# Kernel optimization log

Measured on AMD Instinct MI355X. Metric: run time of the kernel, lower is better.

## Reference

```python
import jax, jax.numpy as jnp
import numpy as np

INPUT, HIDDEN, OUTPUT = 512, 1024, 256
BATCH, SEQ = 128, 512


def setup_inputs() -> dict:
    key = jax.random.key(0)
    ks = jax.random.split(key, 8)
    s_in = 1.0 / np.sqrt(INPUT)
    s_h = 1.0 / np.sqrt(HIDDEN)
    return {
        "x": jax.random.normal(ks[0], (BATCH, SEQ, INPUT), dtype=jnp.float32),
        "W_in": jax.random.uniform(ks[1], (INPUT, HIDDEN), jnp.float32, -s_in, s_in),
        "b_in": jax.random.uniform(ks[2], (HIDDEN,), jnp.float32, -s_in, s_in),
        "W_h": jax.random.uniform(ks[3], (HIDDEN, HIDDEN), jnp.float32, -s_h, s_h),
        "b_h": jax.random.uniform(ks[4], (HIDDEN,), jnp.float32, -s_h, s_h),
        "tau": jnp.ones((HIDDEN,), jnp.float32),
        "W_out": jax.random.uniform(ks[5], (HIDDEN, OUTPUT), jnp.float32, -s_h, s_h),
        "b_out": jax.random.uniform(ks[6], (OUTPUT,), jnp.float32, -s_h, s_h),
    }


def reference(x, W_in, b_in, W_h, b_h, tau, W_out, b_out):
    # Precompute input projections for all timesteps in one big GEMM: [B,S,H]
    xin = jnp.einsum('bsi,ih->bsh', x, W_in) + b_in

    def step(h, xin_t):
        dx = jnp.tanh(xin_t + h @ W_h + b_h)
        h_new = h + (dx - h) / tau
        return h_new, None

    h0 = jnp.zeros((x.shape[0], W_h.shape[0]), x.dtype)
    h_final, _ = jax.lax.scan(step, h0, jnp.swapaxes(xin, 0, 1))
    return h_final @ W_out + b_out
```

## Files before the change

kernel.cpp:

```cpp
#include <hip/hip_runtime.h>
#include <hip/hip_fp16.h>

typedef _Float16 half8 __attribute__((ext_vector_type(8)));
typedef float floatx4 __attribute__((ext_vector_type(4)));
typedef unsigned int uintx4 __attribute__((ext_vector_type(4)));

#define INPUT  512
#define HIDDEN 1024
#define OUTPUT 256
#define BATCH  128
#define SEQ    512

__global__ __launch_bounds__(256) void transpose_f32_to_f16(
    const float* __restrict__ in, _Float16* __restrict__ out, int K, int N) {
  __shared__ float tile[32][33];
  int bi = blockIdx.x;
  int bj = blockIdx.y;
  int cc = threadIdx.x & 31;
  int rr = threadIdx.x >> 5;
#pragma unroll
  for (int s = 0; s < 4; ++s) {
    int r = rr + 8 * s;
    tile[r][cc] = in[(size_t)(bi * 32 + r) * N + bj * 32 + cc];
  }
  __syncthreads();
#pragma unroll
  for (int s = 0; s < 4; ++s) {
    int nl = rr + 8 * s;
    out[(size_t)(bj * 32 + nl) * K + bi * 32 + cc] = (_Float16)tile[cc][nl];
  }
}

__global__ __launch_bounds__(256) void pack_win(
    const float* __restrict__ W, _Float16* __restrict__ P) {
  int idx = blockIdx.x * 256 + threadIdx.x;
  int k = idx >> 10, n = idx & 1023;
  P[((size_t)(k >> 5) << 15) + (n << 5) + (k & 31)] = (_Float16)W[idx];
}

__global__ __launch_bounds__(256) void xin_gemm(
    const float* __restrict__ x, const _Float16* __restrict__ WinP,
    _Float16* __restrict__ xin) {
  int bid = blockIdx.x;
  int bm = (bid & 7) * 128 + ((bid >> 3) & 127);
  int bn = bid >> 10;
  int tid = threadIdx.x;
  int l = tid & 63;
  int w = tid >> 6;
  int l15 = l & 15;
  int lk = (l >> 4) << 3;

  int rowbase = bm * 64 + w * 16;
  int colbase = bn * 128;

  floatx4 acc[8];
#pragma unroll
  for (int nt = 0; nt < 8; ++nt) acc[nt] = (floatx4){0.f, 0.f, 0.f, 0.f};

  const float* xrow = x + (size_t)(rowbase + l15) * INPUT;

  for (int k0 = 0; k0 < INPUT; k0 += 32) {
    int ak = k0 + lk;
    float4 xa = *reinterpret_cast<const float4*>(xrow + ak);
    float4 xb = *reinterpret_cast<const float4*>(xrow + ak + 4);
    half8 a;
    a[0] = (_Float16)xa.x; a[1] = (_Float16)xa.y;
    a[2] = (_Float16)xa.z; a[3] = (_Float16)xa.w;
    a[4] = (_Float16)xb.x; a[5] = (_Float16)xb.y;
    a[6] = (_Float16)xb.z; a[7] = (_Float16)xb.w;
    const _Float16* pq = WinP + ((size_t)(k0 >> 5) << 15) + l15 * 32 + lk;
#pragma unroll
    for (int nt = 0; nt < 8; ++nt) {
      half8 b = *reinterpret_cast<const half8*>(pq + (colbase + nt * 16) * 32);
      acc[nt] = __builtin_amdgcn_mfma_f32_16x16x32_f16(a, b, acc[nt], 0, 0, 0);
    }
  }

  int orow = rowbase + ((l >> 4) << 2);
#pragma unroll
  for (int nt = 0; nt < 8; ++nt)
#pragma unroll
    for (int i = 0; i < 4; ++i) {
      int r = orow + i;
      int b = r >> 9;
      int s = r & 511;
      xin[((size_t)s * BATCH + b) * HIDDEN + colbase + nt * 16 + l15] =
          (_Float16)acc[nt][i];
    }
}

__global__ __launch_bounds__(512) void liquid_scan(
    const _Float16* __restrict__ xin,
    const _Float16* __restrict__ WhT,
    const float* __restrict__ b_in, const float* __restrict__ b_h,
    const float* __restrict__ tau,
    unsigned int* hbuf,
    float* __restrict__ hfinal) {
  int blk = blockIdx.x;
  int m = blk & 7;
  int j = blk >> 3;
  int tid = threadIdx.x;
  int l = tid & 63;
  int w = tid >> 6;
  int nt = w & 3;
  int kg = w >> 2;
  int l15 = l & 15;
  int lk = (l >> 4) << 3;

  __shared__ _Float16 Ald[16][1032];
  __shared__ float part[2][4][2][64];

  int ncol = j * 64 + nt * 16 + l15;
  half8 bfrag[16];
  {
    const _Float16* wb = WhT + (size_t)ncol * HIDDEN + kg * 512 + lk;
#pragma unroll
    for (int q = 0; q < 16; ++q)
      bfrag[q] = *reinterpret_cast<const half8*>(wb + q * 32);
  }

  float bias_c = b_in[ncol] + b_h[ncol];
  float invtau_c = 1.0f / tau[ncol];
  float hown[2] = {0.f, 0.f};
  int erow_i = (l >> 4) << 2;
  const int i0 = kg * 2;
  const int r0 = m * 16 + erow_i + i0;

  const int srow = tid >> 8;
  const int scol4 = (tid & 255) * 4;
  unsigned int* gbase = hbuf + m * 16384 + tid * 4;

  _Float16 xc[2], x1[2], xn[2];
#pragma unroll
  for (int i2 = 0; i2 < 2; ++i2) {
    xc[i2] = xin[((size_t)0 * BATCH + r0 + i2) * HIDDEN + ncol];
    x1[i2] = xin[((size_t)1 * BATCH + r0 + i2) * HIDDEN + ncol];
  }

  for (int t = 0; t < SEQ; ++t) {
    if (t > 0) {
      unsigned int* bp = gbase + (size_t)(t & 1) * 131072;
      const unsigned want = (unsigned)t;
      uintx4 q0, q1, q2, q3, q4, q5, q6, q7;
      for (;;) {
        asm volatile(
            "global_load_dwordx4 %0, %8, off sc1\n\t"
            "global_load_dwordx4 %1, %9, off sc1\n\t"
            "global_load_dwordx4 %2, %10, off sc1\n\t"
            "global_load_dwordx4 %3, %11, off sc1\n\t"
            "global_load_dwordx4 %4, %12, off sc1\n\t"
            "global_load_dwordx4 %5, %13, off sc1\n\t"
            "global_load_dwordx4 %6, %14, off sc1\n\t"
            "global_load_dwordx4 %7, %15, off sc1\n\t"
            "s_waitcnt vmcnt(0)"
            : "=&v"(q0), "=&v"(q1), "=&v"(q2), "=&v"(q3),
              "=&v"(q4), "=&v"(q5), "=&v"(q6), "=&v"(q7)
            : "v"(bp), "v"(bp + 2048), "v"(bp + 4096), "v"(bp + 6144),
              "v"(bp + 8192), "v"(bp + 10240), "v"(bp + 12288),
              "v"(bp + 14336)
            : "memory");
        unsigned bad = 0;
#define CH(Q) bad |= ((Q[0] ^ want) | (Q[1] ^ want) | (Q[2] ^ want) | \
                      (Q[3] ^ want)) & 0xFFFFu;
        CH(q0) CH(q1) CH(q2) CH(q3) CH(q4) CH(q5) CH(q6) CH(q7)
#undef CH
        if (!__any((int)(bad != 0u))) break;
      }
#define STRIP(Q, I)                                                          \
      {                                                                      \
        unsigned lo = __builtin_amdgcn_perm(Q[1], Q[0], 0x07060302u);        \
        unsigned hi = __builtin_amdgcn_perm(Q[3], Q[2], 0x07060302u);        \
        unsigned int* d =                                                    \
            reinterpret_cast<unsigned int*>(&Ald[2 * I + srow][scol4]);      \
        d[0] = lo; d[1] = hi;                                                \
      }
      STRIP(q0, 0) STRIP(q1, 1) STRIP(q2, 2) STRIP(q3, 3)
      STRIP(q4, 4) STRIP(q5, 5) STRIP(q6, 6) STRIP(q7, 7)
#undef STRIP
    }

    {
      int ts = (t + 2 < SEQ) ? t + 2 : SEQ - 1;
      xn[0] = xin[((size_t)ts * BATCH + r0) * HIDDEN + ncol];
      xn[1] = xin[((size_t)ts * BATCH + r0 + 1) * HIDDEN + ncol];
    }
    __syncthreads();

    floatx4 acc = (floatx4){0.f, 0.f, 0.f, 0.f};
    if (t > 0) {
      const int kb = kg * 512 + lk;
#pragma unroll
      for (int q = 0; q < 16; ++q) {
        half8 a = *reinterpret_cast<const half8*>(&Ald[l15][kb + q * 32]);
        acc = __builtin_amdgcn_mfma_f32_16x16x32_f16(a, bfrag[q], acc, 0, 0, 0);
      }
    }
    {
      const int ip = 2 - i0;
#pragma unroll
      for (int i2 = 0; i2 < 2; ++i2) part[1 - kg][nt][i2][l] = acc[ip + i2];
    }
    __syncthreads();

    unsigned int* outb = hbuf + (size_t)((t + 1) & 1) * 131072 + m * 16384;
#pragma unroll
    for (int i2 = 0; i2 < 2; ++i2) {
      float pre = acc[i0 + i2] + part[kg][nt][i2][l] + (float)xc[i2] + bias_c;
      float x2 = fminf(fmaxf(pre, -15.f), 15.f);
      float e = __expf(2.f * x2);
      float dx = (e - 1.f) / (e + 1.f);
      float hn = hown[i2] + (dx - hown[i2]) * invtau_c;
      hown[i2] = hn;
      if (t < SEQ - 1) {
        unsigned short hb = __builtin_bit_cast(unsigned short, (_Float16)hn);
        unsigned word = ((unsigned)hb << 16) | (unsigned)(t + 1);
        __hip_atomic_store(outb + (erow_i + i0 + i2) * 1024 + ncol, word,
                           __ATOMIC_RELAXED, __HIP_MEMORY_SCOPE_AGENT);
      } else {
        hfinal[(size_t)(r0 + i2) * HIDDEN + ncol] = hn;
      }
    }
    xc[0] = x1[0]; xc[1] = x1[1];
    x1[0] = xn[0]; x1[1] = xn[1];
  }
}

__global__ __launch_bounds__(256) void out_gemm(
    const float* __restrict__ hfinal, const float* __restrict__ Wout,
    const float* __restrict__ bout, float* __restrict__ out) {
  int b0 = blockIdx.x * 2;
  int o = threadIdx.x;
  float a0 = 0.f, a1 = 0.f;
  for (int k = 0; k < HIDDEN; ++k) {
    float wv = Wout[(size_t)k * OUTPUT + o];
    a0 += hfinal[(size_t)b0 * HIDDEN + k] * wv;
    a1 += hfinal[(size_t)(b0 + 1) * HIDDEN + k] * wv;
  }
  out[(size_t)b0 * OUTPUT + o] = a0 + bout[o];
  out[(size_t)(b0 + 1) * OUTPUT + o] = a1 + bout[o];
}

extern "C" void kernel_launch(void* const* d_in, const int* in_sizes, int n_in,
                              void* d_out, int out_size, void* d_ws,
                              size_t ws_size, hipStream_t stream) {
  const float* x     = (const float*)d_in[0];
  const float* W_in  = (const float*)d_in[1];
  const float* b_in  = (const float*)d_in[2];
  const float* W_h   = (const float*)d_in[3];
  const float* b_h   = (const float*)d_in[4];
  const float* tau   = (const float*)d_in[5];
  const float* W_out = (const float*)d_in[6];
  const float* b_out = (const float*)d_in[7];
  float* out = (float*)d_out;

  char* ws = (char*)d_ws;
  _Float16* xin = (_Float16*)ws;  ws += (size_t)BATCH * SEQ * HIDDEN * 2;
  _Float16* WinP = (_Float16*)ws; ws += (size_t)INPUT * HIDDEN * 2;
  _Float16* WhT = (_Float16*)ws;  ws += (size_t)HIDDEN * HIDDEN * 2;
  unsigned int* hbuf = (unsigned int*)ws;
  ws += (size_t)2 * BATCH * HIDDEN * 4;
  float* hfin = (float*)ws;       ws += (size_t)BATCH * HIDDEN * 4;

  hipMemsetAsync(hbuf, 0, (size_t)2 * BATCH * HIDDEN * 4, stream);

  transpose_f32_to_f16<<<dim3(HIDDEN / 32, HIDDEN / 32), 256, 0, stream>>>(
      W_h, WhT, HIDDEN, HIDDEN);
  pack_win<<<(INPUT * HIDDEN) / 256, 256, 0, stream>>>(W_in, WinP);

  xin_gemm<<<(BATCH * SEQ / 64) * (HIDDEN / 128), 256, 0, stream>>>(x, WinP,
                                                                    xin);

  liquid_scan<<<128, 512, 0, stream>>>(xin, WhT, b_in, b_h, tau, hbuf, hfin);

  out_gemm<<<BATCH / 2, OUTPUT, 0, stream>>>(hfin, W_out, b_out, out);
}
```

Before: 1.539 ms.

## Split recurrent GEMM over K across waves and poll h directly into registers

The per-step recurrent matmul is restructured so that each of the 8 waves owns a 128-wide K slice and computes all four 16-column N tiles, with the polled hidden-state words unpacked straight into MFMA operands instead of being staged through a shared-memory A tile. The partial sums from the 8 waves are reduced through shared memory, and each thread then finalizes two adjacent columns and publishes them with a single 64-bit atomic store. The input-projection prefetch becomes one 32-bit load holding two halves. This removes the LDS staging of the full h tile and halves the number of flag stores. In exchange it adds an 8-way cross-wave reduction through LDS each step.

```diff
diff --git a/kernel.cpp b/kernel.cpp
--- a/kernel.cpp
+++ b/kernel.cpp
@@ -102,62 +102,64 @@
   int tid = threadIdx.x;
   int l = tid & 63;
   int w = tid >> 6;
-  int nt = w & 3;
-  int kg = w >> 2;
   int l15 = l & 15;
-  int lk = (l >> 4) << 3;
-
-  __shared__ _Float16 Ald[16][1032];
-  __shared__ float part[2][4][2][64];
-
-  int ncol = j * 64 + nt * 16 + l15;
-  half8 bfrag[16];
-  {
-    const _Float16* wb = WhT + (size_t)ncol * HIDDEN + kg * 512 + lk;
-#pragma unroll
-    for (int q = 0; q < 16; ++q)
-      bfrag[q] = *reinterpret_cast<const half8*>(wb + q * 32);
-  }
-
-  float bias_c = b_in[ncol] + b_h[ncol];
-  float invtau_c = 1.0f / tau[ncol];
-  float hown[2] = {0.f, 0.f};
-  int erow_i = (l >> 4) << 2;
-  const int i0 = kg * 2;
-  const int r0 = m * 16 + erow_i + i0;
-
-  const int srow = tid >> 8;
-  const int scol4 = (tid & 255) * 4;
-  unsigned int* gbase = hbuf + m * 16384 + tid * 4;
-
-  _Float16 xc[2], x1[2], xn[2];
-#pragma unroll
-  for (int i2 = 0; i2 < 2; ++i2) {
-    xc[i2] = xin[((size_t)0 * BATCH + r0 + i2) * HIDDEN + ncol];
-    x1[i2] = xin[((size_t)1 * BATCH + r0 + i2) * HIDDEN + ncol];
-  }
+  int hi = l >> 4;
+
+  __shared__ float part_f[8 * 1028];
+
+  half8 wf[4][4];
+#pragma unroll
+  for (int qq = 0; qq < 4; ++qq)
+#pragma unroll
+    for (int nt = 0; nt < 4; ++nt)
+      wf[qq][nt] = *reinterpret_cast<const half8*>(
+          WhT + (size_t)(j * 64 + nt * 16 + l15) * HIDDEN + w * 128 +
+          qq * 32 + hi * 8);
+
+  const int bb = tid >> 5;
+  const int n0 = (tid & 31) * 2;
+  const int gn = j * 64 + n0;
+  const int gb = m * 16 + bb;
+  const float bias0 = b_in[gn] + b_h[gn];
+  const float bias1 = b_in[gn + 1] + b_h[gn + 1];
+  const float it0 = 1.0f / tau[gn];
+  const float it1 = 1.0f / tau[gn + 1];
+  float h0 = 0.f, h1 = 0.f;
+  const int nt_ = n0 >> 4;
+  const int hi_ = (n0 >> 2) & 3;
+  const int i_ = n0 & 3;
+  const int rbase = nt_ * 256 + (bb + (hi_ << 4)) * 4 + i_;
+
+  unsigned int* gpoll = hbuf + m * 16384 + l15 * 1024 + w * 128 + hi * 8;
+
+  const unsigned* xu = reinterpret_cast<const unsigned*>(xin);
+  const size_t xoff = (size_t)gb * 512 + (gn >> 1);
+  unsigned xc = xu[(size_t)0 * 65536 + xoff];
+  unsigned x1v = xu[(size_t)1 * 65536 + xoff];
 
   for (int t = 0; t < SEQ; ++t) {
+    floatx4 acc[4];
+#pragma unroll
+    for (int nt = 0; nt < 4; ++nt) acc[nt] = (floatx4){0.f, 0.f, 0.f, 0.f};
+
     if (t > 0) {
-      unsigned int* bp = gbase + (size_t)(t & 1) * 131072;
+      unsigned int* bp = gpoll + (size_t)(t & 1) * 131072;
       const unsigned want = (unsigned)t;
       uintx4 q0, q1, q2, q3, q4, q5, q6, q7;
       for (;;) {
         asm volatile(
             "global_load_dwordx4 %0, %8, off sc1\n\t"
-            "global_load_dwordx4 %1, %9, off sc1\n\t"
-            "global_load_dwordx4 %2, %10, off sc1\n\t"
-            "global_load_dwordx4 %3, %11, off sc1\n\t"
-            "global_load_dwordx4 %4, %12, off sc1\n\t"
-            "global_load_dwordx4 %5, %13, off sc1\n\t"
-            "global_load_dwordx4 %6, %14, off sc1\n\t"
-            "global_load_dwordx4 %7, %15, off sc1\n\t"
+            "global_load_dwordx4 %1, %8, off offset:16 sc1\n\t"
+            "global_load_dwordx4 %2, %8, off offset:128 sc1\n\t"
+            "global_load_dwordx4 %3, %8, off offset:144 sc1\n\t"
+            "global_load_dwordx4 %4, %8, off offset:256 sc1\n\t"
+            "global_load_dwordx4 %5, %8, off offset:272 sc1\n\t"
+            "global_load_dwordx4 %6, %8, off offset:384 sc1\n\t"
+            "global_load_dwordx4 %7, %8, off offset:400 sc1\n\t"
             "s_waitcnt vmcnt(0)"
             : "=&v"(q0), "=&v"(q1), "=&v"(q2), "=&v"(q3),
               "=&v"(q4), "=&v"(q5), "=&v"(q6), "=&v"(q7)
-            : "v"(bp), "v"(bp + 2048), "v"(bp + 4096), "v"(bp + 6144),
-              "v"(bp + 8192), "v"(bp + 10240), "v"(bp + 12288),
-              "v"(bp + 14336)
+            : "v"(bp)
             : "memory");
         unsigned bad = 0;
 #define CH(Q) bad |= ((Q[0] ^ want) | (Q[1] ^ want) | (Q[2] ^ want) | \
@@ -166,62 +168,84 @@
 #undef CH
         if (!__any((int)(bad != 0u))) break;
       }
-#define STRIP(Q, I)                                                          \
-      {                                                                      \
-        unsigned lo = __builtin_amdgcn_perm(Q[1], Q[0], 0x07060302u);        \
-        unsigned hi = __builtin_amdgcn_perm(Q[3], Q[2], 0x07060302u);        \
-        unsigned int* d =                                                    \
-            reinterpret_cast<unsigned int*>(&Ald[2 * I + srow][scol4]);      \
-        d[0] = lo; d[1] = hi;                                                \
-      }
-      STRIP(q0, 0) STRIP(q1, 1) STRIP(q2, 2) STRIP(q3, 3)
-      STRIP(q4, 4) STRIP(q5, 5) STRIP(q6, 6) STRIP(q7, 7)
-#undef STRIP
-    }
-
-    {
-      int ts = (t + 2 < SEQ) ? t + 2 : SEQ - 1;
-      xn[0] = xin[((size_t)ts * BATCH + r0) * HIDDEN + ncol];
-      xn[1] = xin[((size_t)ts * BATCH + r0 + 1) * HIDDEN + ncol];
-    }
+      uintx4 u;
+      half8 hf[4];
+      u[0] = __builtin_amdgcn_perm(q0[1], q0[0], 0x07060302u);
+      u[1] = __builtin_amdgcn_perm(q0[3], q0[2], 0x07060302u);
+      u[2] = __builtin_amdgcn_perm(q1[1], q1[0], 0x07060302u);
+      u[3] = __builtin_amdgcn_perm(q1[3], q1[2], 0x07060302u);
+      hf[0] = __builtin_bit_cast(half8, u);
+      u[0] = __builtin_amdgcn_perm(q2[1], q2[0], 0x07060302u);
+      u[1] = __builtin_amdgcn_perm(q2[3], q2[2], 0x07060302u);
+      u[2] = __builtin_amdgcn_perm(q3[1], q3[0], 0x07060302u);
+      u[3] = __builtin_amdgcn_perm(q3[3], q3[2], 0x07060302u);
+      hf[1] = __builtin_bit_cast(half8, u);
+      u[0] = __builtin_amdgcn_perm(q4[1], q4[0], 0x07060302u);
+      u[1] = __builtin_amdgcn_perm(q4[3], q4[2], 0x07060302u);
+      u[2] = __builtin_amdgcn_perm(q5[1], q5[0], 0x07060302u);
+      u[3] = __builtin_amdgcn_perm(q5[3], q5[2], 0x07060302u);
+      hf[2] = __builtin_bit_cast(half8, u);
+      u[0] = __builtin_amdgcn_perm(q6[1], q6[0], 0x07060302u);
+      u[1] = __builtin_amdgcn_perm(q6[3], q6[2], 0x07060302u);
+      u[2] = __builtin_amdgcn_perm(q7[1], q7[0], 0x07060302u);
+      u[3] = __builtin_amdgcn_perm(q7[3], q7[2], 0x07060302u);
+      hf[3] = __builtin_bit_cast(half8, u);
+#pragma unroll
+      for (int qq = 0; qq < 4; ++qq)
+#pragma unroll
+        for (int nt = 0; nt < 4; ++nt)
+          acc[nt] = __builtin_amdgcn_mfma_f32_16x16x32_f16(wf[qq][nt], hf[qq],
+                                                           acc[nt], 0, 0, 0);
+    }
+
+    const int ts = (t + 2 < SEQ) ? t + 2 : SEQ - 1;
+    const unsigned xnv = xu[(size_t)ts * 65536 + xoff];
+
+#pragma unroll
+    for (int nt = 0; nt < 4; ++nt)
+      *reinterpret_cast<floatx4*>(&part_f[w * 1028 + nt * 256 + l * 4]) =
+          acc[nt];
     __syncthreads();
 
-    floatx4 acc = (floatx4){0.f, 0.f, 0.f, 0.f};
-    if (t > 0) {
-      const int kb = kg * 512 + lk;
-#pragma unroll
-      for (int q = 0; q < 16; ++q) {
-        half8 a = *reinterpret_cast<const half8*>(&Ald[l15][kb + q * 32]);
-        acc = __builtin_amdgcn_mfma_f32_16x16x32_f16(a, bfrag[q], acc, 0, 0, 0);
-      }
-    }
-    {
-      const int ip = 2 - i0;
-#pragma unroll
-      for (int i2 = 0; i2 < 2; ++i2) part[1 - kg][nt][i2][l] = acc[ip + i2];
+    float s0 = 0.f, s1 = 0.f;
+#pragma unroll
+    for (int k = 0; k < 8; ++k) {
+      const int w2 = (hi_ + k) & 7;
+      const float2 p =
+          *reinterpret_cast<const float2*>(&part_f[w2 * 1028 + rbase]);
+      s0 += p.x; s1 += p.y;
     }
     __syncthreads();
 
-    unsigned int* outb = hbuf + (size_t)((t + 1) & 1) * 131072 + m * 16384;
-#pragma unroll
-    for (int i2 = 0; i2 < 2; ++i2) {
-      float pre = acc[i0 + i2] + part[kg][nt][i2][l] + (float)xc[i2] + bias_c;
-      float x2 = fminf(fmaxf(pre, -15.f), 15.f);
-      float e = __expf(2.f * x2);
-      float dx = (e - 1.f) / (e + 1.f);
-      float hn = hown[i2] + (dx - hown[i2]) * invtau_c;
-      hown[i2] = hn;
-      if (t < SEQ - 1) {
-        unsigned short hb = __builtin_bit_cast(unsigned short, (_Float16)hn);
-        unsigned word = ((unsigned)hb << 16) | (unsigned)(t + 1);
-        __hip_atomic_store(outb + (erow_i + i0 + i2) * 1024 + ncol, word,
-                           __ATOMIC_RELAXED, __HIP_MEMORY_SCOPE_AGENT);
-      } else {
-        hfinal[(size_t)(r0 + i2) * HIDDEN + ncol] = hn;
-      }
-    }
-    xc[0] = x1[0]; xc[1] = x1[1];
-    x1[0] = xn[0]; x1[1] = xn[1];
+    const float xv0 =
+        (float)__builtin_bit_cast(_Float16, (unsigned short)(xc & 0xFFFFu));
+    const float xv1 =
+        (float)__builtin_bit_cast(_Float16, (unsigned short)(xc >> 16));
+    float pre0 = s0 + xv0 + bias0;
+    float pre1 = s1 + xv1 + bias1;
+    pre0 = fminf(fmaxf(pre0, -15.f), 15.f);
+    pre1 = fminf(fmaxf(pre1, -15.f), 15.f);
+    const float e0 = __expf(2.f * pre0), e1 = __expf(2.f * pre1);
+    const float dx0 = (e0 - 1.f) / (e0 + 1.f), dx1 = (e1 - 1.f) / (e1 + 1.f);
+    h0 += (dx0 - h0) * it0;
+    h1 += (dx1 - h1) * it1;
+
+    if (t < SEQ - 1) {
+      const unsigned short hb0 = __builtin_bit_cast(unsigned short, (_Float16)h0);
+      const unsigned short hb1 = __builtin_bit_cast(unsigned short, (_Float16)h1);
+      const unsigned w0 = ((unsigned)hb0 << 16) | (unsigned)(t + 1);
+      const unsigned w1 = ((unsigned)hb1 << 16) | (unsigned)(t + 1);
+      const unsigned long long dw = (unsigned long long)w0 |
+                                    ((unsigned long long)w1 << 32);
+      unsigned long long* p = reinterpret_cast<unsigned long long*>(
+          hbuf + (size_t)((t + 1) & 1) * 131072 + m * 16384 + bb * 1024 + gn);
+      __hip_atomic_store(p, dw, __ATOMIC_RELAXED, __HIP_MEMORY_SCOPE_AGENT);
+    } else {
+      *reinterpret_cast<float2*>(&hfinal[(size_t)gb * HIDDEN + gn]) =
+          (float2){h0, h1};
+    }
+    xc = x1v;
+    x1v = xnv;
   }
 }
 
```

Result: slower. 2.111 ms (+37.2%).

## Halve scan block to 4 waves with two MFMA tiles each and per-chunk polling

Applied to the files above, without the earlier changes.

The recurrent scan kernel now runs 256 threads per block instead of 512. Each wave holds two 16-column weight fragments and issues two MFMA chains per K-step. The global h exchange buffer is relaid so each thread reads 16 contiguous 16-byte chunks through one base pointer. Polling now retries only the chunks whose timestamps are stale rather than reloading everything. The aim is to cut sync and handshake overhead and improve MFMA ILP, at the cost of more registers per thread and fewer waves to hide latency.

```diff
diff --git a/kernel.cpp b/kernel.cpp
--- a/kernel.cpp
+++ b/kernel.cpp
@@ -89,7 +89,7 @@
     }
 }
 
-__global__ __launch_bounds__(512) void liquid_scan(
+__global__ __launch_bounds__(256) void liquid_scan(
     const _Float16* __restrict__ xin,
     const _Float16* __restrict__ WhT,
     const float* __restrict__ b_in, const float* __restrict__ b_h,
@@ -102,126 +102,164 @@
   int tid = threadIdx.x;
   int l = tid & 63;
   int w = tid >> 6;
-  int nt = w & 3;
-  int kg = w >> 2;
+  int p = w & 1;
+  int kg = w >> 1;
   int l15 = l & 15;
-  int lk = (l >> 4) << 3;
+  int hi = l >> 4;
+  int lk = hi << 3;
 
   __shared__ _Float16 Ald[16][1032];
-  __shared__ float part[2][4][2][64];
-
-  int ncol = j * 64 + nt * 16 + l15;
-  half8 bfrag[16];
+  __shared__ float part[2][2][4][64];
+
+  half8 wf0[16], wf1[16];
   {
-    const _Float16* wb = WhT + (size_t)ncol * HIDDEN + kg * 512 + lk;
-#pragma unroll
-    for (int q = 0; q < 16; ++q)
-      bfrag[q] = *reinterpret_cast<const half8*>(wb + q * 32);
-  }
-
-  float bias_c = b_in[ncol] + b_h[ncol];
-  float invtau_c = 1.0f / tau[ncol];
-  float hown[2] = {0.f, 0.f};
-  int erow_i = (l >> 4) << 2;
-  const int i0 = kg * 2;
-  const int r0 = m * 16 + erow_i + i0;
-
-  const int srow = tid >> 8;
-  const int scol4 = (tid & 255) * 4;
-  unsigned int* gbase = hbuf + m * 16384 + tid * 4;
-
-  _Float16 xc[2], x1[2], xn[2];
-#pragma unroll
-  for (int i2 = 0; i2 < 2; ++i2) {
-    xc[i2] = xin[((size_t)0 * BATCH + r0 + i2) * HIDDEN + ncol];
-    x1[i2] = xin[((size_t)1 * BATCH + r0 + i2) * HIDDEN + ncol];
+    const _Float16* wb0 =
+        WhT + (size_t)(j * 64 + p * 32 + l15) * HIDDEN + kg * 512 + lk;
+    const _Float16* wb1 = wb0 + 16 * HIDDEN;
+#pragma unroll
+    for (int q = 0; q < 16; ++q) {
+      wf0[q] = *reinterpret_cast<const half8*>(wb0 + q * 32);
+      wf1[q] = *reinterpret_cast<const half8*>(wb1 + q * 32);
+    }
+  }
+
+  const int c = j * 64 + p * 32 + kg * 16 + l15;
+  const float bias_c = b_in[c] + b_h[c];
+  const float invtau_c = 1.0f / tau[c];
+  float hown[4] = {0.f, 0.f, 0.f, 0.f};
+  const int gb0 = m * 16 + hi * 4;
+  const int Wbase = (c >> 2) * 64 + (c & 3);
+
+  _Float16 xc[4], x1[4], xn[4];
+#pragma unroll
+  for (int i = 0; i < 4; ++i) {
+    xc[i] = xin[((size_t)0 * BATCH + gb0 + i) * HIDDEN + c];
+    x1[i] = xin[((size_t)1 * BATCH + gb0 + i) * HIDDEN + c];
   }
 
   for (int t = 0; t < SEQ; ++t) {
     if (t > 0) {
-      unsigned int* bp = gbase + (size_t)(t & 1) * 131072;
+      unsigned int* bp =
+          hbuf + (size_t)(t & 1) * 131072 + m * 16384 + tid * 64;
       const unsigned want = (unsigned)t;
-      uintx4 q0, q1, q2, q3, q4, q5, q6, q7;
-      for (;;) {
-        asm volatile(
-            "global_load_dwordx4 %0, %8, off sc1\n\t"
-            "global_load_dwordx4 %1, %9, off sc1\n\t"
-            "global_load_dwordx4 %2, %10, off sc1\n\t"
-            "global_load_dwordx4 %3, %11, off sc1\n\t"
-            "global_load_dwordx4 %4, %12, off sc1\n\t"
-            "global_load_dwordx4 %5, %13, off sc1\n\t"
-            "global_load_dwordx4 %6, %14, off sc1\n\t"
-            "global_load_dwordx4 %7, %15, off sc1\n\t"
-            "s_waitcnt vmcnt(0)"
-            : "=&v"(q0), "=&v"(q1), "=&v"(q2), "=&v"(q3),
-              "=&v"(q4), "=&v"(q5), "=&v"(q6), "=&v"(q7)
-            : "v"(bp), "v"(bp + 2048), "v"(bp + 4096), "v"(bp + 6144),
-              "v"(bp + 8192), "v"(bp + 10240), "v"(bp + 12288),
-              "v"(bp + 14336)
-            : "memory");
-        unsigned bad = 0;
-#define CH(Q) bad |= ((Q[0] ^ want) | (Q[1] ^ want) | (Q[2] ^ want) | \
-                      (Q[3] ^ want)) & 0xFFFFu;
-        CH(q0) CH(q1) CH(q2) CH(q3) CH(q4) CH(q5) CH(q6) CH(q7)
-#undef CH
-        if (!__any((int)(bad != 0u))) break;
-      }
+      uintx4 q0, q1, q2, q3, q4, q5, q6, q7, q8, q9, qa, qb, qc, qd, qe, qf;
+      asm volatile(
+          "global_load_dwordx4 %0, %16, off sc1\n\t"
+          "global_load_dwordx4 %1, %16, off offset:16 sc1\n\t"
+          "global_load_dwordx4 %2, %16, off offset:32 sc1\n\t"
+          "global_load_dwordx4 %3, %16, off offset:48 sc1\n\t"
+          "global_load_dwordx4 %4, %16, off offset:64 sc1\n\t"
+          "global_load_dwordx4 %5, %16, off offset:80 sc1\n\t"
+          "global_load_dwordx4 %6, %16, off offset:96 sc1\n\t"
+          "global_load_dwordx4 %7, %16, off offset:112 sc1\n\t"
+          "global_load_dwordx4 %8, %16, off offset:128 sc1\n\t"
+          "global_load_dwordx4 %9, %16, off offset:144 sc1\n\t"
+          "global_load_dwordx4 %10, %16, off offset:160 sc1\n\t"
+          "global_load_dwordx4 %11, %16, off offset:176 sc1\n\t"
+          "global_load_dwordx4 %12, %16, off offset:192 sc1\n\t"
+          "global_load_dwordx4 %13, %16, off offset:208 sc1\n\t"
+          "global_load_dwordx4 %14, %16, off offset:224 sc1\n\t"
+          "global_load_dwordx4 %15, %16, off offset:240 sc1\n\t"
+          "s_waitcnt vmcnt(0)"
+          : "=&v"(q0), "=&v"(q1), "=&v"(q2), "=&v"(q3), "=&v"(q4),
+            "=&v"(q5), "=&v"(q6), "=&v"(q7), "=&v"(q8), "=&v"(q9),
+            "=&v"(qa), "=&v"(qb), "=&v"(qc), "=&v"(qd), "=&v"(qe),
+            "=&v"(qf)
+          : "v"(bp)
+          : "memory");
+      unsigned need = 0u;
+#define CHK(Q, I)                                                         \
+      {                                                                   \
+        unsigned bad = ((Q[0] ^ want) | (Q[1] ^ want) | (Q[2] ^ want) |   \
+                        (Q[3] ^ want)) & 0xFFFFu;                         \
+        if (__any(bad != 0u)) need |= (1u << I);                          \
+      }
+      CHK(q0, 0) CHK(q1, 1) CHK(q2, 2) CHK(q3, 3) CHK(q4, 4) CHK(q5, 5)
+      CHK(q6, 6) CHK(q7, 7) CHK(q8, 8) CHK(q9, 9) CHK(qa, 10) CHK(qb, 11)
+      CHK(qc, 12) CHK(qd, 13) CHK(qe, 14) CHK(qf, 15)
+      while (need) {
+#define RETRY(Q, I, OFF)                                                  \
+        if (need & (1u << I)) {                                           \
+          asm volatile("global_load_dwordx4 %0, %1, off offset:" #OFF     \
+                       " sc1\n\ts_waitcnt vmcnt(0)"                       \
+                       : "=&v"(Q) : "v"(bp) : "memory");                  \
+          unsigned bad = ((Q[0] ^ want) | (Q[1] ^ want) | (Q[2] ^ want) | \
+                          (Q[3] ^ want)) & 0xFFFFu;                       \
+          if (!__any(bad != 0u)) need &= ~(1u << I);                      \
+        }
+        RETRY(q0, 0, 0) RETRY(q1, 1, 16) RETRY(q2, 2, 32) RETRY(q3, 3, 48)
+        RETRY(q4, 4, 64) RETRY(q5, 5, 80) RETRY(q6, 6, 96) RETRY(q7, 7, 112)
+        RETRY(q8, 8, 128) RETRY(q9, 9, 144) RETRY(qa, 10, 160)
+        RETRY(qb, 11, 176) RETRY(qc, 12, 192) RETRY(qd, 13, 208)
+        RETRY(qe, 14, 224) RETRY(qf, 15, 240)
+#undef RETRY
+      }
+#undef CHK
 #define STRIP(Q, I)                                                          \
       {                                                                      \
         unsigned lo = __builtin_amdgcn_perm(Q[1], Q[0], 0x07060302u);        \
-        unsigned hi = __builtin_amdgcn_perm(Q[3], Q[2], 0x07060302u);        \
+        unsigned hi2 = __builtin_amdgcn_perm(Q[3], Q[2], 0x07060302u);       \
         unsigned int* d =                                                    \
-            reinterpret_cast<unsigned int*>(&Ald[2 * I + srow][scol4]);      \
-        d[0] = lo; d[1] = hi;                                                \
-      }
-      STRIP(q0, 0) STRIP(q1, 1) STRIP(q2, 2) STRIP(q3, 3)
-      STRIP(q4, 4) STRIP(q5, 5) STRIP(q6, 6) STRIP(q7, 7)
+            reinterpret_cast<unsigned int*>(&Ald[I][tid * 4]);               \
+        d[0] = lo; d[1] = hi2;                                               \
+      }
+      STRIP(q0, 0) STRIP(q1, 1) STRIP(q2, 2) STRIP(q3, 3) STRIP(q4, 4)
+      STRIP(q5, 5) STRIP(q6, 6) STRIP(q7, 7) STRIP(q8, 8) STRIP(q9, 9)
+      STRIP(qa, 10) STRIP(qb, 11) STRIP(qc, 12) STRIP(qd, 13) STRIP(qe, 14)
+      STRIP(qf, 15)
 #undef STRIP
     }
 
     {
-      int ts = (t + 2 < SEQ) ? t + 2 : SEQ - 1;
-      xn[0] = xin[((size_t)ts * BATCH + r0) * HIDDEN + ncol];
-      xn[1] = xin[((size_t)ts * BATCH + r0 + 1) * HIDDEN + ncol];
+      const int ts = (t + 2 < SEQ) ? t + 2 : SEQ - 1;
+#pragma unroll
+      for (int i = 0; i < 4; ++i)
+        xn[i] = xin[((size_t)ts * BATCH + gb0 + i) * HIDDEN + c];
     }
     __syncthreads();
 
-    floatx4 acc = (floatx4){0.f, 0.f, 0.f, 0.f};
+    floatx4 acc0 = (floatx4){0.f, 0.f, 0.f, 0.f};
+    floatx4 acc1 = (floatx4){0.f, 0.f, 0.f, 0.f};
     if (t > 0) {
       const int kb = kg * 512 + lk;
 #pragma unroll
       for (int q = 0; q < 16; ++q) {
         half8 a = *reinterpret_cast<const half8*>(&Ald[l15][kb + q * 32]);
-        acc = __builtin_amdgcn_mfma_f32_16x16x32_f16(a, bfrag[q], acc, 0, 0, 0);
-      }
-    }
-    {
-      const int ip = 2 - i0;
-#pragma unroll
-      for (int i2 = 0; i2 < 2; ++i2) part[1 - kg][nt][i2][l] = acc[ip + i2];
+        acc0 = __builtin_amdgcn_mfma_f32_16x16x32_f16(a, wf0[q], acc0, 0, 0, 0);
+        acc1 = __builtin_amdgcn_mfma_f32_16x16x32_f16(a, wf1[q], acc1, 0, 0, 0);
+      }
+    }
+    if (kg == 0) {
+#pragma unroll
+      for (int i = 0; i < 4; ++i) part[p][1][i][l] = acc1[i];
+    } else {
+#pragma unroll
+      for (int i = 0; i < 4; ++i) part[p][0][i][l] = acc0[i];
     }
     __syncthreads();
 
     unsigned int* outb = hbuf + (size_t)((t + 1) & 1) * 131072 + m * 16384;
 #pragma unroll
-    for (int i2 = 0; i2 < 2; ++i2) {
-      float pre = acc[i0 + i2] + part[kg][nt][i2][l] + (float)xc[i2] + bias_c;
-      float x2 = fminf(fmaxf(pre, -15.f), 15.f);
-      float e = __expf(2.f * x2);
-      float dx = (e - 1.f) / (e + 1.f);
-      float hn = hown[i2] + (dx - hown[i2]) * invtau_c;
-      hown[i2] = hn;
+    for (int i = 0; i < 4; ++i) {
+      const float mine = (kg == 0) ? acc0[i] : acc1[i];
+      float pre = mine + part[p][kg][i][l] + (float)xc[i] + bias_c;
+      pre = fminf(fmaxf(pre, -15.f), 15.f);
+      const float e = __expf(2.f * pre);
+      const float dx = (e - 1.f) / (e + 1.f);
+      const float hn = hown[i] + (dx - hown[i]) * invtau_c;
+      hown[i] = hn;
       if (t < SEQ - 1) {
-        unsigned short hb = __builtin_bit_cast(unsigned short, (_Float16)hn);
-        unsigned word = ((unsigned)hb << 16) | (unsigned)(t + 1);
-        __hip_atomic_store(outb + (erow_i + i0 + i2) * 1024 + ncol, word,
+        const unsigned short hb =
+            __builtin_bit_cast(unsigned short, (_Float16)hn);
+        const unsigned word = ((unsigned)hb << 16) | (unsigned)(t + 1);
+        __hip_atomic_store(outb + Wbase + (hi * 4 + i) * 4, word,
                            __ATOMIC_RELAXED, __HIP_MEMORY_SCOPE_AGENT);
       } else {
-        hfinal[(size_t)(r0 + i2) * HIDDEN + ncol] = hn;
-      }
-    }
-    xc[0] = x1[0]; xc[1] = x1[1];
-    x1[0] = xn[0]; x1[1] = xn[1];
+        hfinal[(size_t)(gb0 + i) * HIDDEN + c] = hn;
+      }
+    }
+#pragma unroll
+    for (int i = 0; i < 4; ++i) { xc[i] = x1[i]; x1[i] = xn[i]; }
   }
 }
 
@@ -270,7 +308,7 @@
   xin_gemm<<<(BATCH * SEQ / 64) * (HIDDEN / 128), 256, 0, stream>>>(x, WinP,
                                                                     xin);
 
-  liquid_scan<<<128, 512, 0, stream>>>(xin, WhT, b_in, b_h, tau, hbuf, hfin);
+  liquid_scan<<<128, 256, 0, stream>>>(xin, WhT, b_in, b_h, tau, hbuf, hfin);
 
   out_gemm<<<BATCH / 2, OUTPUT, 0, stream>>>(hfin, W_out, b_out, out);
 }
```

Result: slower. 3.249 ms (+111.1%).

## Split recurrent GEMM K across four waves with shared-memory reduction

Applied to the files above, without the earlier changes.

Each wave in the persistent scan now covers 32 output columns over a quarter of K (256), where before it covered 16 columns over half of K. Each A fragment loaded from LDS feeds two MFMAs, so LDS reads per wave drop and the MFMA chain per wave is shorter. The four partial sums go into a rearranged shared buffer, and each thread then reduces four partials for its own two batch rows when computing the element-wise update. The cost is more LDS writes and a 4-way reduction, and the epilogue thread-to-column mapping changes, so the xin and hbuf address patterns differ.

```diff
diff --git a/kernel.cpp b/kernel.cpp
--- a/kernel.cpp
+++ b/kernel.cpp
@@ -102,29 +102,41 @@
   int tid = threadIdx.x;
   int l = tid & 63;
   int w = tid >> 6;
-  int nt = w & 3;
-  int kg = w >> 2;
+  int g = w & 1;
+  int kg = w >> 1;
   int l15 = l & 15;
   int lk = (l >> 4) << 3;
 
   __shared__ _Float16 Ald[16][1032];
-  __shared__ float part[2][4][2][64];
-
-  int ncol = j * 64 + nt * 16 + l15;
-  half8 bfrag[16];
+  __shared__ float part[2][2][4][64][4];
+
+  half8 wf0[8], wf1[8];
   {
-    const _Float16* wb = WhT + (size_t)ncol * HIDDEN + kg * 512 + lk;
-#pragma unroll
-    for (int q = 0; q < 16; ++q)
-      bfrag[q] = *reinterpret_cast<const half8*>(wb + q * 32);
-  }
-
-  float bias_c = b_in[ncol] + b_h[ncol];
-  float invtau_c = 1.0f / tau[ncol];
+    const _Float16* wb0 =
+        WhT + (size_t)(j * 64 + g * 32 + l15) * HIDDEN + kg * 256 + lk;
+    const _Float16* wb1 = wb0 + 16 * HIDDEN;
+#pragma unroll
+    for (int kt = 0; kt < 8; ++kt) {
+      wf0[kt] = *reinterpret_cast<const half8*>(wb0 + kt * 32);
+      wf1[kt] = *reinterpret_cast<const half8*>(wb1 + kt * 32);
+    }
+  }
+
+  const int wp = tid >> 6;
+  const int lp = tid & 63;
+  const int gc = j * 64 + lp;
+  const float bias_c = b_in[gc] + b_h[gc];
+  const float invtau_c = 1.0f / tau[gc];
   float hown[2] = {0.f, 0.f};
-  int erow_i = (l >> 4) << 2;
-  const int i0 = kg * 2;
-  const int r0 = m * 16 + erow_i + i0;
+  const int r0 = 2 * wp;
+  const int gb0 = m * 16 + r0;
+
+  const int ntg = lp >> 5;
+  const int nt2 = (lp >> 4) & 1;
+  const int lsrc0 = (((r0 + 0) >> 2) << 4) | (lp & 15);
+  const int lsrc1 = (((r0 + 1) >> 2) << 4) | (lp & 15);
+  const int i_0 = (r0 + 0) & 3;
+  const int i_1 = (r0 + 1) & 3;
 
   const int srow = tid >> 8;
   const int scol4 = (tid & 255) * 4;
@@ -132,9 +144,9 @@
 
   _Float16 xc[2], x1[2], xn[2];
 #pragma unroll
-  for (int i2 = 0; i2 < 2; ++i2) {
-    xc[i2] = xin[((size_t)0 * BATCH + r0 + i2) * HIDDEN + ncol];
-    x1[i2] = xin[((size_t)1 * BATCH + r0 + i2) * HIDDEN + ncol];
+  for (int b = 0; b < 2; ++b) {
+    xc[b] = xin[((size_t)0 * BATCH + gb0 + b) * HIDDEN + gc];
+    x1[b] = xin[((size_t)1 * BATCH + gb0 + b) * HIDDEN + gc];
   }
 
   for (int t = 0; t < SEQ; ++t) {
@@ -180,44 +192,53 @@
     }
 
     {
-      int ts = (t + 2 < SEQ) ? t + 2 : SEQ - 1;
-      xn[0] = xin[((size_t)ts * BATCH + r0) * HIDDEN + ncol];
-      xn[1] = xin[((size_t)ts * BATCH + r0 + 1) * HIDDEN + ncol];
+      const int ts = (t + 2 < SEQ) ? t + 2 : SEQ - 1;
+      xn[0] = xin[((size_t)ts * BATCH + gb0) * HIDDEN + gc];
+      xn[1] = xin[((size_t)ts * BATCH + gb0 + 1) * HIDDEN + gc];
     }
     __syncthreads();
 
-    floatx4 acc = (floatx4){0.f, 0.f, 0.f, 0.f};
+    floatx4 acc0 = (floatx4){0.f, 0.f, 0.f, 0.f};
+    floatx4 acc1 = (floatx4){0.f, 0.f, 0.f, 0.f};
     if (t > 0) {
-      const int kb = kg * 512 + lk;
-#pragma unroll
-      for (int q = 0; q < 16; ++q) {
-        half8 a = *reinterpret_cast<const half8*>(&Ald[l15][kb + q * 32]);
-        acc = __builtin_amdgcn_mfma_f32_16x16x32_f16(a, bfrag[q], acc, 0, 0, 0);
+      const int kb = kg * 256 + lk;
+#pragma unroll
+      for (int kt = 0; kt < 8; ++kt) {
+        half8 a = *reinterpret_cast<const half8*>(&Ald[l15][kb + kt * 32]);
+        acc0 = __builtin_amdgcn_mfma_f32_16x16x32_f16(a, wf0[kt], acc0, 0, 0, 0);
+        acc1 = __builtin_amdgcn_mfma_f32_16x16x32_f16(a, wf1[kt], acc1, 0, 0, 0);
       }
     }
     {
-      const int ip = 2 - i0;
-#pragma unroll
-      for (int i2 = 0; i2 < 2; ++i2) part[1 - kg][nt][i2][l] = acc[ip + i2];
+      const int slot = (kg + (l >> 3)) & 3;
+#pragma unroll
+      for (int i = 0; i < 4; ++i) {
+        part[g][0][i][l][slot] = acc0[i];
+        part[g][1][i][l][slot] = acc1[i];
+      }
     }
     __syncthreads();
 
     unsigned int* outb = hbuf + (size_t)((t + 1) & 1) * 131072 + m * 16384;
 #pragma unroll
-    for (int i2 = 0; i2 < 2; ++i2) {
-      float pre = acc[i0 + i2] + part[kg][nt][i2][l] + (float)xc[i2] + bias_c;
-      float x2 = fminf(fmaxf(pre, -15.f), 15.f);
-      float e = __expf(2.f * x2);
-      float dx = (e - 1.f) / (e + 1.f);
-      float hn = hown[i2] + (dx - hown[i2]) * invtau_c;
-      hown[i2] = hn;
+    for (int b = 0; b < 2; ++b) {
+      const floatx4 p = *reinterpret_cast<const floatx4*>(
+          &part[ntg][nt2][b ? i_1 : i_0][b ? lsrc1 : lsrc0][0]);
+      const float s = (p[0] + p[1]) + (p[2] + p[3]);
+      float pre = s + (float)xc[b] + bias_c;
+      pre = fminf(fmaxf(pre, -15.f), 15.f);
+      const float e = __expf(2.f * pre);
+      const float dx = (e - 1.f) / (e + 1.f);
+      const float hn = hown[b] + (dx - hown[b]) * invtau_c;
+      hown[b] = hn;
       if (t < SEQ - 1) {
-        unsigned short hb = __builtin_bit_cast(unsigned short, (_Float16)hn);
-        unsigned word = ((unsigned)hb << 16) | (unsigned)(t + 1);
-        __hip_atomic_store(outb + (erow_i + i0 + i2) * 1024 + ncol, word,
+        const unsigned short hb =
+            __builtin_bit_cast(unsigned short, (_Float16)hn);
+        const unsigned word = ((unsigned)hb << 16) | (unsigned)(t + 1);
+        __hip_atomic_store(outb + (r0 + b) * 1024 + gc, word,
                            __ATOMIC_RELAXED, __HIP_MEMORY_SCOPE_AGENT);
       } else {
-        hfinal[(size_t)(r0 + i2) * HIDDEN + ncol] = hn;
+        hfinal[(size_t)(gb0 + b) * HIDDEN + gc] = hn;
       }
     }
     xc[0] = x1[0]; xc[1] = x1[1];
```

Result: faster. 1.408 ms (-8.5%).
